# Performance work log

Hardware: AMD Instinct MI355X
Metric: run time of the kernel (lower is better)

The kernel has to match this reference:

```python
import math
import jax, jax.numpy as jnp
import numpy as np
from jax import lax

BIG = 1e20
HUGE = 1e30
SMALL = 1e-10
EPSILON = 0.1
NITER = 50
B, I, J = 256, 256, 256


def setup_inputs() -> dict:
    key = jax.random.key(0)
    # normalized word-pair distances in [0, 1)
    D = jax.random.uniform(key, (B, I, J), dtype=jnp.float32)
    return {"D": D}


def _kl_div(x, y):
    div = x / (y + SMALL)
    return y * (div * jnp.log(div + SMALL) - div + 1.0)


def _wfr_forward(D, epsilon, niter):
    pi2 = jnp.float32(math.pi / 2)
    C = -2.0 * jnp.log(jnp.cos(jnp.minimum(D * 2.0, pi2)) + 1e-5)  # [B,I,J]
    b_, i_, j_ = C.shape
    dx = 1.0 / i_  # uniform weights 1/I
    dy = 1.0 / j_  # uniform weights 1/J
    p_coef = 1.0 / (1.0 + epsilon)

    def K_calc(u, v):
        # K = clamp(exp((-C + u_i + v_j)/eps))
        return jnp.clip(jnp.exp((-C + u[:, :, None] + v[:, None, :]) / epsilon), 0.0, HUGE)

    b0 = jnp.ones((b_, j_), C.dtype)
    u0 = jnp.zeros((b_, i_), C.dtype)
    v0 = jnp.zeros((b_, j_), C.dtype)
    K0 = K_calc(u0, v0)

    def body(ii, carry):
        b, u, v, K = carry
        # row update: s_i = sum_j K_ij * b_j * dy ; mu = 1
        s = jnp.sum(K * (b * dy)[:, None, :], axis=-1)  # [B,I]
        a = jnp.clip((1.0 / (jnp.exp(u) * s)) ** p_coef, 0.0, HUGE)
        # col update: s_j = sum_i K_ij * a_i * dx ; nu = 1
        s2 = jnp.sum(K * (a * dx)[:, :, None], axis=-2)  # [B,J]
        b_new = jnp.clip((1.0 / (jnp.exp(v) * s2)) ** p_coef, 0.0, HUGE)

        rescale = (jnp.max(a) > BIG) | (jnp.max(b_new) > BIG) | (ii == niter - 1)

        def do_rescale(_):
            u2 = epsilon * jnp.log(a) + u
            v2 = epsilon * jnp.log(b_new) + v
            return jnp.ones_like(b_new), u2, v2, K_calc(u2, v2)

        def no_rescale(_):
            return b_new, u, v, K

        return lax.cond(rescale, do_rescale, no_rescale, None)

    b, u, v, K = lax.fori_loop(0, niter, body, (b0, u0, v0, K0))

    # marginal constraint penalties (KL against uniform mu=nu=1)
    row_marg = jnp.sum(K * dy, axis=-1)            # [B,I]
    cons1 = jnp.sum(_kl_div(row_marg, 1.0) * dx, axis=-1)
    col_marg = jnp.sum(K * dx, axis=-2)            # [B,J]
    cons2 = jnp.sum(_kl_div(col_marg, 1.0) * dy, axis=-1)
    transport = jnp.sum(K * C, axis=(-2, -1)) * dx * dy
    p_opt = cons1 + cons2 + transport               # [B]
    return p_opt, K


def reference(D):
    p_opt, _K = _wfr_forward(D, EPSILON, NITER)
    return p_opt
```

## Files before the change

kernel.cpp:

```cpp
#include <hip/hip_runtime.h>
#include <hip/hip_fp16.h>
#include <math.h>

#define NITERS 50

typedef _Float16 h2_t __attribute__((ext_vector_type(2)));

#if defined(__has_builtin)
#if __has_builtin(__builtin_amdgcn_fdot2)
#define HAVE_FDOT2 1
#endif
#endif

__device__ __forceinline__ float fdot2f(unsigned int ka, unsigned int kb, float acc) {
#ifdef HAVE_FDOT2
    return __builtin_amdgcn_fdot2(__builtin_bit_cast(h2_t, ka),
                                  __builtin_bit_cast(h2_t, kb), acc, false);
#else
    h2_t a = __builtin_bit_cast(h2_t, ka);
    h2_t b = __builtin_bit_cast(h2_t, kb);
    return acc + (float)a.x * (float)b.x + (float)a.y * (float)b.y;
#endif
}

__global__ __launch_bounds__(512) void wfr_kernel(const float* __restrict__ D,
                                                  float* __restrict__ out) {
    __shared__ __align__(16) __half Ksh[256 * 256];
    __shared__ __align__(16) float  sh_bf[256];
    __shared__ __align__(16) float  sh_af[256];
    __shared__ __align__(16) float  sh_s2[256];
    __shared__ __align__(16) __half sh_bh[256];
    __shared__ __align__(16) float  part[512];
    __shared__ __align__(16) float  cpart[4096];

    const int tid = threadIdx.x;
    const int bb  = blockIdx.x;
    char* Kbytes  = reinterpret_cast<char*>(Ksh);

    {
        const float4* D4 = reinterpret_cast<const float4*>(D + (size_t)bb * 65536);
        for (int k = 0; k < 32; ++k) {
            int idx4 = tid + (k << 9);
            float4 d = D4[idx4];
            int i = idx4 >> 6;
            int j = (idx4 & 63) << 2;
            float v0[4] = {d.x, d.y, d.z, d.w};
            float k0[4];
            #pragma unroll
            for (int q = 0; q < 4; ++q) {
                float c = cosf(fminf(v0[q] * 2.0f, 1.57079632679489662f)) + 1e-5f;
                k0[q] = expf(20.0f * logf(c));
            }
            h2_t h01 = { (_Float16)k0[0], (_Float16)k0[1] };
            h2_t h23 = { (_Float16)k0[2], (_Float16)k0[3] };
            uint2 wv;
            wv.x = __builtin_bit_cast(unsigned int, h01);
            wv.y = __builtin_bit_cast(unsigned int, h23);
            int off = (i << 9) + (((j << 1) ^ ((i & 31) << 4)));
            *reinterpret_cast<uint2*>(Kbytes + off) = wv;
        }
    }
    if (tid < 256) {
        sh_bf[tid] = 1.0f;
        sh_bh[tid] = __float2half(1.0f);
    }
    __syncthreads();

    const int r   = tid & 255;
    const int hh  = tid >> 8;
    const int rsw = r & 31;
    const char* Krow = Kbytes + (r << 9);
    const int g   = tid & 31;
    const int hc  = tid >> 5;

    for (int it = 0; it < NITERS; ++it) {
        float s = 0.0f;
        #pragma unroll
        for (int c = 0; c < 16; ++c) {
            int chunk = (hh << 4) + c;
            uint4 kv = *reinterpret_cast<const uint4*>(Krow + ((chunk ^ rsw) << 4));
            uint4 bv = *reinterpret_cast<const uint4*>(
                reinterpret_cast<const char*>(sh_bh) + (chunk << 4));
            s = fdot2f(kv.x, bv.x, s);
            s = fdot2f(kv.y, bv.y, s);
            s = fdot2f(kv.z, bv.z, s);
            s = fdot2f(kv.w, bv.w, s);
        }
        part[tid] = s;
        __syncthreads();
        if (tid < 256) {
            float sf = (part[tid] + part[tid + 256]) * (1.0f / 256.0f);
            float a  = __powf(1.0f / sf, 1.0f / 1.1f);
            a = fminf(a, 1e30f);
            sh_af[tid] = a;
        }
        __syncthreads();

        float f0=0,f1=0,f2=0,f3=0,f4=0,f5=0,f6=0,f7=0;
        #pragma unroll
        for (int m = 0; m < 16; ++m) {
            int i = (hc << 4) + m;
            float ai = sh_af[i];
            uint4 kv = *reinterpret_cast<const uint4*>(
                Kbytes + (i << 9) + ((g ^ (i & 31)) << 4));
            h2_t p0 = __builtin_bit_cast(h2_t, kv.x);
            h2_t p1 = __builtin_bit_cast(h2_t, kv.y);
            h2_t p2 = __builtin_bit_cast(h2_t, kv.z);
            h2_t p3 = __builtin_bit_cast(h2_t, kv.w);
            f0 = fmaf((float)p0.x, ai, f0);
            f1 = fmaf((float)p0.y, ai, f1);
            f2 = fmaf((float)p1.x, ai, f2);
            f3 = fmaf((float)p1.y, ai, f3);
            f4 = fmaf((float)p2.x, ai, f4);
            f5 = fmaf((float)p2.y, ai, f5);
            f6 = fmaf((float)p3.x, ai, f6);
            f7 = fmaf((float)p3.y, ai, f7);
        }
        {
            float* cp = cpart + (hc << 8) + (g << 3);
            *reinterpret_cast<float4*>(cp)     = make_float4(f0, f1, f2, f3);
            *reinterpret_cast<float4*>(cp + 4) = make_float4(f4, f5, f6, f7);
        }
        __syncthreads();
        if (tid < 256) {
            float s2 = 0.0f;
            #pragma unroll
            for (int q = 0; q < 16; ++q) s2 += cpart[(q << 8) + tid];
            s2 *= (1.0f / 256.0f);
            float bn = __powf(1.0f / s2, 1.0f / 1.1f);
            bn = fminf(bn, 1e30f);
            sh_bf[tid] = bn;
            sh_bh[tid] = __float2half(bn);
            sh_s2[tid] = s2;
        }
        __syncthreads();
    }

    {
        float s = 0.0f, tp = 0.0f;
        #pragma unroll
        for (int c = 0; c < 16; ++c) {
            int chunk = (hh << 4) + c;
            uint4 kv = *reinterpret_cast<const uint4*>(Krow + ((chunk ^ rsw) << 4));
            float4 blo = *reinterpret_cast<const float4*>(sh_bf + (chunk << 3));
            float4 bhi = *reinterpret_cast<const float4*>(sh_bf + (chunk << 3) + 4);
            h2_t p0 = __builtin_bit_cast(h2_t, kv.x);
            h2_t p1 = __builtin_bit_cast(h2_t, kv.y);
            h2_t p2 = __builtin_bit_cast(h2_t, kv.z);
            h2_t p3 = __builtin_bit_cast(h2_t, kv.w);
            float kf[8] = {(float)p0.x,(float)p0.y,(float)p1.x,(float)p1.y,
                           (float)p2.x,(float)p2.y,(float)p3.x,(float)p3.y};
            float bf[8] = {blo.x,blo.y,blo.z,blo.w,bhi.x,bhi.y,bhi.z,bhi.w};
            #pragma unroll
            for (int q = 0; q < 8; ++q) {
                float prod = kf[q] * bf[q];
                s += prod;
                float cl = (kf[q] > 0.0f) ? (-0.1f * __logf(kf[q])) : 0.0f;
                tp = fmaf(prod, cl, tp);
            }
        }
        part[tid]  = s;
        cpart[tid] = tp;
    }
    __syncthreads();
    float val = 0.0f;
    if (tid < 256) {
        float sfin     = (part[tid] + part[tid + 256]) * (1.0f / 256.0f);
        float af       = sh_af[tid];
        float row_marg = af * sfin;
        float col_marg = sh_bf[tid] * sh_s2[tid];
        float tprow    = af * (cpart[tid] + cpart[tid + 256]);
        float d1  = row_marg / (1.0f + 1e-10f);
        float kl1 = d1 * __logf(d1 + 1e-10f) - d1 + 1.0f;
        float d2  = col_marg / (1.0f + 1e-10f);
        float kl2 = d2 * __logf(d2 + 1e-10f) - d2 + 1.0f;
        val = (kl1 + kl2) * (1.0f / 256.0f) + tprow * (1.0f / 65536.0f);
    }
    __syncthreads();
    part[tid] = val;
    __syncthreads();
    for (int off = 256; off > 0; off >>= 1) {
        if (tid < off) part[tid] += part[tid + off];
        __syncthreads();
    }
    if (tid == 0) out[bb] = part[0];
}

extern "C" void kernel_launch(void* const* d_in, const int* in_sizes, int n_in,
                              void* d_out, int out_size, void* d_ws, size_t ws_size,
                              hipStream_t stream) {
    (void)in_sizes; (void)n_in; (void)d_ws; (void)ws_size; (void)out_size;
    const float* D = reinterpret_cast<const float*>(d_in[0]);
    float* out     = reinterpret_cast<float*>(d_out);
    wfr_kernel<<<dim3(256), dim3(512), 0, stream>>>(D, out);
}
```

Baseline: 238.9 us.

## Cache each thread's K row and column slices in registers across iterations

Each thread now loads its 16 row chunks and 16 column chunks of K from LDS into registers once, before the Sinkhorn loop, and reuses them in all 50 iterations and the final reduction. This removes repeated LDS reads of K, leaving only the small b/a vector reads per iteration. It also splits the row dot product into four independent accumulators and sets the launch bound to min 2 blocks. Holding 128 extra VGPRs per thread risks register pressure or spilling at 512 threads. The 2-blocks hint cannot raise occupancy because each block uses about 150KB of LDS.

Measured after the change: 204.5 us. 1.17x faster.

```diff
diff --git a/kernel.cpp b/kernel.cpp
--- a/kernel.cpp
+++ b/kernel.cpp
@@ -23,8 +23,8 @@
 #endif
 }
 
-__global__ __launch_bounds__(512) void wfr_kernel(const float* __restrict__ D,
-                                                  float* __restrict__ out) {
+__global__ __launch_bounds__(512, 2) void wfr_kernel(const float* __restrict__ D,
+                                                     float* __restrict__ out) {
     __shared__ __align__(16) __half Ksh[256 * 256];
     __shared__ __align__(16) float  sh_bf[256];
     __shared__ __align__(16) float  sh_af[256];
@@ -73,20 +73,32 @@
     const int g   = tid & 31;
     const int hc  = tid >> 5;
 
+    uint4 krow4[16];
+    #pragma unroll
+    for (int c = 0; c < 16; ++c) {
+        int chunk = (hh << 4) + c;
+        krow4[c] = *reinterpret_cast<const uint4*>(Krow + ((chunk ^ rsw) << 4));
+    }
+    uint4 kcol4[16];
+    #pragma unroll
+    for (int m = 0; m < 16; ++m) {
+        int i = (hc << 4) + m;
+        kcol4[m] = *reinterpret_cast<const uint4*>(
+            Kbytes + (i << 9) + ((g ^ (i & 31)) << 4));
+    }
+
     for (int it = 0; it < NITERS; ++it) {
-        float s = 0.0f;
+        float s0 = 0.0f, s1 = 0.0f, s2a = 0.0f, s3 = 0.0f;
         #pragma unroll
         for (int c = 0; c < 16; ++c) {
-            int chunk = (hh << 4) + c;
-            uint4 kv = *reinterpret_cast<const uint4*>(Krow + ((chunk ^ rsw) << 4));
             uint4 bv = *reinterpret_cast<const uint4*>(
-                reinterpret_cast<const char*>(sh_bh) + (chunk << 4));
-            s = fdot2f(kv.x, bv.x, s);
-            s = fdot2f(kv.y, bv.y, s);
-            s = fdot2f(kv.z, bv.z, s);
-            s = fdot2f(kv.w, bv.w, s);
-        }
-        part[tid] = s;
+                reinterpret_cast<const char*>(sh_bh) + (((hh << 4) + c) << 4));
+            s0  = fdot2f(krow4[c].x, bv.x, s0);
+            s1  = fdot2f(krow4[c].y, bv.y, s1);
+            s2a = fdot2f(krow4[c].z, bv.z, s2a);
+            s3  = fdot2f(krow4[c].w, bv.w, s3);
+        }
+        part[tid] = (s0 + s1) + (s2a + s3);
         __syncthreads();
         if (tid < 256) {
             float sf = (part[tid] + part[tid + 256]) * (1.0f / 256.0f);
@@ -99,14 +111,11 @@
         float f0=0,f1=0,f2=0,f3=0,f4=0,f5=0,f6=0,f7=0;
         #pragma unroll
         for (int m = 0; m < 16; ++m) {
-            int i = (hc << 4) + m;
-            float ai = sh_af[i];
-            uint4 kv = *reinterpret_cast<const uint4*>(
-                Kbytes + (i << 9) + ((g ^ (i & 31)) << 4));
-            h2_t p0 = __builtin_bit_cast(h2_t, kv.x);
-            h2_t p1 = __builtin_bit_cast(h2_t, kv.y);
-            h2_t p2 = __builtin_bit_cast(h2_t, kv.z);
-            h2_t p3 = __builtin_bit_cast(h2_t, kv.w);
+            float ai = sh_af[(hc << 4) + m];
+            h2_t p0 = __builtin_bit_cast(h2_t, kcol4[m].x);
+            h2_t p1 = __builtin_bit_cast(h2_t, kcol4[m].y);
+            h2_t p2 = __builtin_bit_cast(h2_t, kcol4[m].z);
+            h2_t p3 = __builtin_bit_cast(h2_t, kcol4[m].w);
             f0 = fmaf((float)p0.x, ai, f0);
             f1 = fmaf((float)p0.y, ai, f1);
             f2 = fmaf((float)p1.x, ai, f2);
@@ -141,13 +150,12 @@
         #pragma unroll
         for (int c = 0; c < 16; ++c) {
             int chunk = (hh << 4) + c;
-            uint4 kv = *reinterpret_cast<const uint4*>(Krow + ((chunk ^ rsw) << 4));
             float4 blo = *reinterpret_cast<const float4*>(sh_bf + (chunk << 3));
             float4 bhi = *reinterpret_cast<const float4*>(sh_bf + (chunk << 3) + 4);
-            h2_t p0 = __builtin_bit_cast(h2_t, kv.x);
-            h2_t p1 = __builtin_bit_cast(h2_t, kv.y);
-            h2_t p2 = __builtin_bit_cast(h2_t, kv.z);
-            h2_t p3 = __builtin_bit_cast(h2_t, kv.w);
+            h2_t p0 = __builtin_bit_cast(h2_t, krow4[c].x);
+            h2_t p1 = __builtin_bit_cast(h2_t, krow4[c].y);
+            h2_t p2 = __builtin_bit_cast(h2_t, krow4[c].z);
+            h2_t p3 = __builtin_bit_cast(h2_t, krow4[c].w);
             float kf[8] = {(float)p0.x,(float)p0.y,(float)p1.x,(float)p1.y,
                            (float)p2.x,(float)p2.y,(float)p3.x,(float)p3.y};
             float bf[8] = {blo.x,blo.y,blo.z,blo.w,bhi.x,bhi.y,bhi.z,bhi.w};
```
